# Kernel optimization log

Hardware: AMD Instinct MI355X
Metric: run time of the kernel (lower is better)

The kernel has to match this reference:

```python
import jax, jax.numpy as jnp
import numpy as np

B, T, C = 2, 2048, 2048
N_HEAD = 16
HD = C // N_HEAD  # 128


def setup_inputs() -> dict:
    key = jax.random.key(0)
    k1, k2, k3, k4, k5 = jax.random.split(key, 5)
    s_in = 1.0 / np.sqrt(C)
    return {
        "x": jax.random.normal(k1, (B, T, C), dtype=jnp.float32),
        # weights stored as (in, out), i.e. transpose of torch Linear weight
        "W_attn": jax.random.normal(k2, (C, 3 * C), dtype=jnp.float32) * s_in,
        "b_attn": jax.random.normal(k3, (3 * C,), dtype=jnp.float32) * 0.02,
        "W_proj": jax.random.normal(k4, (C, C), dtype=jnp.float32) * s_in,
        "b_proj": jax.random.normal(k5, (C,), dtype=jnp.float32) * 0.02,
    }


def reference(x, W_attn, b_attn, W_proj, b_proj):
    # qkv projection: (B,T,3C)
    qkv = x @ W_attn + b_attn
    q, k, v = jnp.split(qkv, 3, axis=-1)
    # (B, n_head, T, head_dim)
    q = q.reshape(B, T, N_HEAD, HD).transpose(0, 2, 1, 3)
    k = k.reshape(B, T, N_HEAD, HD).transpose(0, 2, 1, 3)
    v = v.reshape(B, T, N_HEAD, HD).transpose(0, 2, 1, 3)
    # scores (B,H,T,T), causal mask (T_q == T_k prefill path)
    att = jnp.einsum("bhqd,bhkd->bhqk", q, k) * (1.0 / np.sqrt(HD))
    causal = jnp.tril(jnp.ones((T, T), dtype=bool))
    att = jnp.where(causal[None, None], att, -jnp.inf)
    att = jax.nn.softmax(att, axis=-1)  # attn_dropout is identity (p=0)
    y = jnp.einsum("bhqk,bhkd->bhqd", att, v)
    y = y.transpose(0, 2, 1, 3).reshape(B, T, C)
    y = y @ W_proj + b_proj  # resid_dropout identity (p=0)
    # new_cache = (k, v, T) since T == block_size; return output tensor
    return y
```

## Files before the change

### kernel.cpp

```cpp
#include <hip/hip_runtime.h>
#include <cstdint>
#include <cstddef>


typedef __bf16 bf16x8 __attribute__((ext_vector_type(8)));
typedef float  f32x4  __attribute__((ext_vector_type(4)));
typedef unsigned short u16x4 __attribute__((ext_vector_type(4)));
typedef unsigned short u16x8 __attribute__((ext_vector_type(8)));

__device__ __forceinline__ unsigned short f2bf(float f) {
  unsigned int u = __builtin_bit_cast(unsigned int, f);
  u += 0x7fffu + ((u >> 16) & 1u);
  return (unsigned short)(u >> 16);
}

__device__ __forceinline__ void gld16(void* lds, const void* g) {
  __builtin_amdgcn_global_load_lds(
      (const __attribute__((address_space(1))) void*)g,
      (__attribute__((address_space(3))) void*)lds, 16, 0, 0);
}

__device__ __forceinline__ unsigned lds_addr(const void* p) {
  return (unsigned)(size_t)(const __attribute__((address_space(3))) void*)p;
}

__device__ __forceinline__ bf16x8 ds_read16(unsigned addr) {
  bf16x8 r;
  asm volatile("ds_read_b128 %0, %1" : "=v"(r) : "v"(addr));
  return r;
}

__device__ __forceinline__ void ds_write8(unsigned addr, u16x4 d) {
  unsigned long long v = __builtin_bit_cast(unsigned long long, d);
  asm volatile("ds_write_b64 %0, %1" :: "v"(addr), "v"(v));
}

__device__ __forceinline__ void transpose_tile_64(
    const float* __restrict__ in, unsigned short* __restrict__ out,
    int R, int C, int c0, int r0, int t, float tile[64][65]) {
  int lr = t >> 4, lc = (t & 15) * 4;
#pragma unroll
  for (int i = 0; i < 4; i++) {
    int row = lr + i * 16;
    float4 v = *(const float4*)&in[(size_t)(r0 + row) * C + c0 + lc];
    tile[row][lc] = v.x; tile[row][lc + 1] = v.y;
    tile[row][lc + 2] = v.z; tile[row][lc + 3] = v.w;
  }
  __syncthreads();
  int wr = t >> 3, wc = (t & 7) * 8;
#pragma unroll
  for (int i = 0; i < 2; i++) {
    int crow = wr + i * 32;
    u16x8 o;
#pragma unroll
    for (int j = 0; j < 8; j++) o[j] = f2bf(tile[wc + j][crow]);
    *(u16x8*)&out[(size_t)(c0 + crow) * R + r0 + wc] = o;
  }
}

__global__ __launch_bounds__(256) void prep_k(
    const float* __restrict__ x, const float* __restrict__ W_attn,
    const float* __restrict__ W_proj, unsigned short* __restrict__ x_bf,
    unsigned short* __restrict__ WaT, unsigned short* __restrict__ WpT) {
  __shared__ float tile[64][65];
  const int bid = blockIdx.x, t = threadIdx.x;
  if (bid < 3072) {
    int bx = bid % 96, by = bid / 96;
    transpose_tile_64(W_attn, WaT, 2048, 6144, bx * 64, by * 64, t, tile);
  } else if (bid < 4096) {
    int id = bid - 3072, bx = id & 31, by = id >> 5;
    transpose_tile_64(W_proj, WpT, 2048, 2048, bx * 64, by * 64, t, tile);
  } else {
    const int n4 = 8388608 / 4;
    int i = (bid - 4096) * 256 + t;
    for (; i < n4; i += 1024 * 256) {
      float4 v = ((const float4*)x)[i];
      ushort4 o;
      o.x = f2bf(v.x); o.y = f2bf(v.y); o.z = f2bf(v.z); o.w = f2bf(v.w);
      ((ushort4*)x_bf)[i] = o;
    }
  }
}

__global__ __launch_bounds__(256) void extract_vT_k(
    const unsigned short* __restrict__ qkv, unsigned short* __restrict__ vT) {
  __shared__ unsigned int tile32[64][33];
  int bh = blockIdx.z, b = bh >> 4, h = bh & 15;
  int t0 = blockIdx.x * 64, d0 = blockIdx.y * 64;
  int t = threadIdx.x;
  int lr = t >> 3, lc = (t & 7) * 8;
  const unsigned short* src = qkv + (size_t)(b * 2048) * 6144 + 4096 + h * 128;
#pragma unroll
  for (int i = 0; i < 2; i++) {
    int row = lr + i * 32;
    u16x8 v = *(const u16x8*)&src[(size_t)(t0 + row) * 6144 + d0 + lc];
#pragma unroll
    for (int j = 0; j < 8; j++) {
      unsigned short* p = (unsigned short*)&tile32[lc + j][row & 31];
      p[row >> 5] = v[j];
    }
  }
  __syncthreads();
  int dr = t >> 2, tc = (t & 3) * 8;
  u16x8 lo, hi;
#pragma unroll
  for (int j = 0; j < 8; j++) {
    unsigned int u = tile32[dr][tc + j];
    lo[j] = (unsigned short)(u & 0xffffu);
    hi[j] = (unsigned short)(u >> 16);
  }
  unsigned short* dst = vT + (size_t)bh * 128 * 2048 + (size_t)(d0 + dr) * 2048 + t0;
  *(u16x8*)&dst[tc] = lo;
  *(u16x8*)&dst[tc + 32] = hi;
}

template <int OUT_BF16>
__global__ __launch_bounds__(256) void gemm_bt(
    const unsigned short* __restrict__ A, const unsigned short* __restrict__ BT,
    const float* __restrict__ bias, void* __restrict__ Cout,
    int M, int N, int K) {
  __shared__ __align__(16) unsigned short sA[128 * 64];
  __shared__ __align__(16) unsigned short sB[128 * 64];

  const int tid = threadIdx.x, w = tid >> 6, lane = tid & 63;
  const int quad = lane >> 4, l16 = lane & 15;
  const int m0 = blockIdx.y * 128, n0 = blockIdx.x * 128;
  const int wr = w >> 1, wc = w & 1;

  const unsigned short* gA[4];
  const unsigned short* gB[4];
  unsigned short* lA[4];
  unsigned short* lB[4];
#pragma unroll
  for (int i = 0; i < 4; i++) {
    int c = w * 256 + i * 64 + lane;
    int row = c >> 3, scol = (c & 7) ^ (row & 7);
    gA[i] = A + (size_t)(m0 + row) * K + scol * 8;
    gB[i] = BT + (size_t)(n0 + row) * K + scol * 8;
    lA[i] = sA + (size_t)(w * 256 + i * 64) * 8;
    lB[i] = sB + (size_t)(w * 256 + i * 64) * 8;
  }

  f32x4 acc[4][4] = {};

  for (int k0 = 0; k0 < K; k0 += 64) {
#pragma unroll
    for (int i = 0; i < 4; i++) {
      gld16(lA[i], gA[i]); gld16(lB[i], gB[i]);
      gA[i] += 64; gB[i] += 64;
    }
    __syncthreads();

#pragma unroll
    for (int kk = 0; kk < 2; kk++) {
      const int cc = (kk * 4 + quad) ^ (l16 & 7);
      bf16x8 af[4], bfr[4];
#pragma unroll
      for (int mi = 0; mi < 4; mi++)
        af[mi] = *(const bf16x8*)&sA[(wr * 64 + mi * 16 + l16) * 64 + cc * 8];
#pragma unroll
      for (int ni = 0; ni < 4; ni++)
        bfr[ni] = *(const bf16x8*)&sB[(wc * 64 + ni * 16 + l16) * 64 + cc * 8];
#pragma unroll
      for (int mi = 0; mi < 4; mi++)
#pragma unroll
        for (int ni = 0; ni < 4; ni++)
          acc[mi][ni] = __builtin_amdgcn_mfma_f32_16x16x32_bf16(
              af[mi], bfr[ni], acc[mi][ni], 0, 0, 0);
    }
    __syncthreads();
  }

#pragma unroll
  for (int mi = 0; mi < 4; mi++) {
    int row = m0 + wr * 64 + mi * 16 + quad * 4;
#pragma unroll
    for (int ni = 0; ni < 4; ni++) {
      int col = n0 + wc * 64 + ni * 16 + l16;
      float bv = bias[col];
#pragma unroll
      for (int r = 0; r < 4; r++) {
        float v = acc[mi][ni][r] + bv;
        if (OUT_BF16)
          ((unsigned short*)Cout)[(size_t)(row + r) * N + col] = f2bf(v);
        else
          ((float*)Cout)[(size_t)(row + r) * N + col] = v;
      }
    }
  }
}

#define BARRIER8 __builtin_amdgcn_s_barrier()
#define WAIT_LGKM0 asm volatile("s_waitcnt lgkmcnt(0)" ::: "memory")
#define WAIT_LGKM4 asm volatile("s_waitcnt lgkmcnt(4)" ::: "memory")
#define WAIT_LGKM5 asm volatile("s_waitcnt lgkmcnt(5)" ::: "memory")
#define SCHED0 __builtin_amdgcn_sched_barrier(0)
#define WAIT_VM4 asm volatile("s_waitcnt vmcnt(4)" ::: "memory")
#define WAIT_VM0 asm volatile("s_waitcnt vmcnt(0)" ::: "memory")

#define STAGE_A(buf, h, t)                                                   \
  do {                                                                       \
    gld16(&sA[buf][((h) * 1024 + w * 64) * 8],                               \
          gA0 + (size_t)(h) * 128 * K + (size_t)(t) * 64);                   \
    gld16(&sA[buf][((h) * 1024 + 512 + w * 64) * 8],                         \
          gA1 + (size_t)(h) * 128 * K + (size_t)(t) * 64);                   \
  } while (0)

#define STAGE_B(buf, h, t)                                                   \
  do {                                                                       \
    gld16(&sB[buf][((h) * 1024 + w * 64) * 8],                               \
          gB0 + (size_t)(h) * 128 * K + (size_t)(t) * 64);                   \
    gld16(&sB[buf][((h) * 1024 + 512 + w * 64) * 8],                         \
          gB1 + (size_t)(h) * 128 * K + (size_t)(t) * 64);                   \
  } while (0)

#define LDA4(buf, mh, kk)                                                    \
  do {                                                                       \
    const int cc_ = ((kk) * 4 + quad) ^ (l16 & 7);                           \
    _Pragma("unroll") for (int i_ = 0; i_ < 4; ++i_) {                       \
      const int rr_ = (mh) * 128 + wr * 64 + i_ * 16 + l16;                  \
      a_[i_] = ds_read16(lds_addr(&sA[buf][rr_ * 64 + cc_ * 8]));            \
    }                                                                        \
  } while (0)

#define LDB4(buf, kk)                                                        \
  do {                                                                       \
    const int cc_ = ((kk) * 4 + quad) ^ (l16 & 7);                           \
    _Pragma("unroll") for (int i_ = 0; i_ < 4; ++i_) {                       \
      const int rr_ = wc * 64 + i_ * 16 + l16;                               \
      b_[i_] = ds_read16(lds_addr(&sB[buf][rr_ * 64 + cc_ * 8]));            \
    }                                                                        \
  } while (0)

#define MM16(mh)                                                             \
  do {                                                                       \
    __builtin_amdgcn_s_setprio(1);                                           \
    _Pragma("unroll") for (int i_ = 0; i_ < 4; ++i_)                         \
    _Pragma("unroll") for (int n_ = 0; n_ < 4; ++n_)                         \
        acc[(mh) * 4 + i_][n_] = __builtin_amdgcn_mfma_f32_16x16x32_bf16(    \
            a_[i_], b_[n_], acc[(mh) * 4 + i_][n_], 0, 0, 0);                \
    __builtin_amdgcn_s_setprio(0);                                           \
  } while (0)

template <int OUT_BF16>
__global__ __launch_bounds__(512, 2) void gemm_bt8(
    const unsigned short* __restrict__ A, const unsigned short* __restrict__ BT,
    const float* __restrict__ bias, void* __restrict__ Cout,
    int M, int N, int K) {
  __shared__ __align__(16) unsigned short sA[2][256 * 64];
  __shared__ __align__(16) unsigned short sB[2][256 * 64];
  (void)M;

  const int tid = threadIdx.x, w = tid >> 6, lane = tid & 63;
  const int quad = lane >> 4, l16 = lane & 15;
  const int wr = w >> 2, wc = w & 3;

  const int nwgx = gridDim.x;
  const int nwg = nwgx * gridDim.y;
  const int wg = blockIdx.y * nwgx + blockIdx.x;
  const int q8 = nwg >> 3, r8 = nwg & 7;
  const int xcd = wg & 7, loc = wg >> 3;
  const int swz =
      (xcd < r8 ? xcd * (q8 + 1) : r8 * (q8 + 1) + (xcd - r8) * q8) + loc;
  const int m0 = (swz / nwgx) * 256;
  const int n0 = (swz % nwgx) * 256;

  const int c0 = tid, c1 = tid + 512;
  const int r0c = c0 >> 3, s0c = (c0 & 7) ^ (r0c & 7);
  const int r1c = c1 >> 3, s1c = (c1 & 7) ^ (r1c & 7);
  const unsigned short* gA0 = A + (size_t)(m0 + r0c) * K + s0c * 8;
  const unsigned short* gA1 = A + (size_t)(m0 + r1c) * K + s1c * 8;
  const unsigned short* gB0 = BT + (size_t)(n0 + r0c) * K + s0c * 8;
  const unsigned short* gB1 = BT + (size_t)(n0 + r1c) * K + s1c * 8;

  f32x4 acc[8][4] = {};
  bf16x8 a_[4], b_[4];

  const int NT = K >> 6;
  const int NI = NT >> 1;

  STAGE_B(0, 0, 0); STAGE_A(0, 0, 0);
  STAGE_B(0, 1, 0); STAGE_A(0, 1, 0);
  STAGE_B(1, 0, 1); STAGE_A(1, 0, 1);
  WAIT_VM4;
  BARRIER8;

  for (int i = 0; i < NI; ++i) {
    const int t1 = 2 * i + 1;
    const int tn0 = 2 * i + 2, tn1 = 2 * i + 3;
    const bool last = (i == NI - 1);

    LDB4(0, 0); LDA4(0, 0, 0);
    STAGE_B(1, 1, t1); STAGE_A(1, 1, t1);
    BARRIER8; WAIT_LGKM0; SCHED0; MM16(0); BARRIER8;

    LDA4(0, 1, 0);
    BARRIER8; WAIT_LGKM0; SCHED0; MM16(1); BARRIER8;

    LDB4(0, 1); LDA4(0, 0, 1);
    BARRIER8; WAIT_LGKM0; SCHED0; MM16(0); BARRIER8;

    LDA4(0, 1, 1);
    if (!last) {
      STAGE_B(0, 0, tn0); STAGE_A(0, 0, tn0);
      WAIT_VM4;
    } else {
      WAIT_VM0;
    }
    BARRIER8; WAIT_LGKM0; SCHED0; MM16(1); BARRIER8;

    LDB4(1, 0); LDA4(1, 0, 0);
    if (!last) { STAGE_B(0, 1, tn0); STAGE_A(0, 1, tn0); }
    BARRIER8; WAIT_LGKM0; SCHED0; MM16(0); BARRIER8;

    LDA4(1, 1, 0);
    BARRIER8; WAIT_LGKM0; SCHED0; MM16(1); BARRIER8;

    LDB4(1, 1); LDA4(1, 0, 1);
    BARRIER8; WAIT_LGKM0; SCHED0; MM16(0); BARRIER8;

    LDA4(1, 1, 1);
    if (!last) {
      STAGE_B(1, 0, tn1); STAGE_A(1, 0, tn1);
      WAIT_VM4;
    }
    BARRIER8; WAIT_LGKM0; SCHED0; MM16(1); BARRIER8;
  }

#pragma unroll
  for (int mi = 0; mi < 8; ++mi) {
    const int mh = mi >> 2, i2 = mi & 3;
    int row = m0 + mh * 128 + wr * 64 + i2 * 16 + quad * 4;
#pragma unroll
    for (int ni = 0; ni < 4; ++ni) {
      int col = n0 + wc * 64 + ni * 16 + l16;
      float bv = bias[col];
#pragma unroll
      for (int rr = 0; rr < 4; ++rr) {
        float v = acc[mi][ni][rr] + bv;
        if (OUT_BF16)
          ((unsigned short*)Cout)[(size_t)(row + rr) * N + col] = f2bf(v);
        else
          ((float*)Cout)[(size_t)(row + rr) * N + col] = v;
      }
    }
  }
}

#undef STAGE_A
#undef STAGE_B
#undef LDA4
#undef LDB4
#undef MM16

__global__ __launch_bounds__(256) void flash_attn(
    const unsigned short* __restrict__ qkv, const unsigned short* __restrict__ vT,
    unsigned short* __restrict__ yout) {
  __shared__ __align__(16) unsigned short sK[2][64 * 128];
  __shared__ __align__(16) unsigned short sVT[2][128 * 64];
  __shared__ __align__(16) unsigned short sP[4 * 16 * 64];

  const int tid = threadIdx.x, w = tid >> 6, lane = tid & 63;
  const int quad = lane >> 4, l16 = lane & 15;
  const int id = blockIdx.x;
  const int g = id & 31;
  const int qp = id >> 5;
  const int b = g >> 4, h = g & 15;
  const int T = 2048, CC = 6144, HD = 128;
  const float qscale = 0.12753257252f;

  const unsigned short* gK = qkv + (size_t)(b * T) * CC + 2048 + h * HD;
  const unsigned short* gV = vT + (size_t)(b * 16 + h) * HD * T;
  unsigned short* pw = sP + w * 16 * 64;

  const unsigned short* kSrc[4];
  const unsigned short* vSrc[4];
  unsigned short* kDst[4];
  unsigned short* vDst[4];
#pragma unroll
  for (int i = 0; i < 4; i++) {
    int c = w * 256 + i * 64 + lane;
    int kR = c >> 4, kC = (c & 15) ^ (kR & 15);
    int vR = c >> 3, vC = (c & 7) ^ (vR & 7);
    kSrc[i] = gK + (size_t)kR * CC + kC * 8;
    vSrc[i] = gV + (size_t)vR * T + vC * 8;
    kDst[i] = (unsigned short*)sK + (size_t)(w * 256 + i * 64) * 8;
    vDst[i] = (unsigned short*)sVT + (size_t)(w * 256 + i * 64) * 8;
  }
  const int KBUF = 64 * 128, VBUF = 128 * 64;

  const int qtA = qp, qtB = 31 - qp;
  int qt = qtA, kt = 0;

  bf16x8 qf[4];
  float m_old, l_sum;
  f32x4 o[8] = {};
  {
    const size_t qrow = (size_t)(b * T + qt * 64 + w * 16 + l16) * CC + h * HD;
#pragma unroll
    for (int kb = 0; kb < 4; kb++) {
      bf16x8 raw = *(const bf16x8*)&qkv[qrow + kb * 32 + quad * 8];
      bf16x8 sc;
#pragma unroll
      for (int j = 0; j < 8; j++) sc[j] = (__bf16)((float)raw[j] * qscale);
      qf[kb] = sc;
    }
  }
  m_old = -1e30f; l_sum = 0.f;

#pragma unroll
  for (int i = 0; i < 4; i++) {
    gld16(kDst[i], kSrc[i]);
    gld16(vDst[i], vSrc[i]);
  }

  const int total = qtA + qtB + 2;
  for (int it = 0; it < total; ++it) {
    __syncthreads();
    const int cur = it & 1;
    const bool segEnd = (kt == qt);

    if (it + 1 < total) {
      const int nkt = segEnd ? 0 : kt + 1;
      const int nb_ = (it + 1) & 1;
      const size_t kOff = (size_t)nkt * 64 * CC;
      const int vOff = nkt * 64;
#pragma unroll
      for (int i = 0; i < 4; i++) {
        gld16(kDst[i] + (size_t)nb_ * KBUF, kSrc[i] + kOff);
        gld16(vDst[i] + (size_t)nb_ * VBUF, vSrc[i] + vOff);
      }
    }

    const unsigned short* sKc = (const unsigned short*)sK + (size_t)cur * KBUF;
    const unsigned short* sVc = (const unsigned short*)sVT + (size_t)cur * VBUF;

    f32x4 s4[4] = {};
    bf16x8 kf[4], kg[4];
#pragma unroll
    for (int kb = 0; kb < 4; kb++) {
      int rr = kb * 16 + l16;
      int cc = quad ^ l16;
      kf[kb] = ds_read16(lds_addr(&sKc[rr * 128 + cc * 8]));
    }
#pragma unroll
    for (int dc = 0; dc < 4; dc++) {
      if (dc < 3) {
#pragma unroll
        for (int kb = 0; kb < 4; kb++) {
          int rr = kb * 16 + l16;
          int cc = ((dc + 1) * 4 + quad) ^ l16;
          kg[kb] = ds_read16(lds_addr(&sKc[rr * 128 + cc * 8]));
        }
        WAIT_LGKM4;
      } else {
        WAIT_LGKM0;
      }
      SCHED0;
      __builtin_amdgcn_s_setprio(1);
#pragma unroll
      for (int kb = 0; kb < 4; kb++)
        s4[kb] = __builtin_amdgcn_mfma_f32_16x16x32_bf16(kf[kb], qf[dc], s4[kb], 0, 0, 0);
      __builtin_amdgcn_s_setprio(0);
      if (dc < 3) {
#pragma unroll
        for (int kb = 0; kb < 4; kb++) kf[kb] = kg[kb];
      }
    }

    float sv[4][4];
#pragma unroll
    for (int kb = 0; kb < 4; kb++)
#pragma unroll
      for (int r = 0; r < 4; r++) {
        float v = s4[kb][r];
        if (segEnd) {
          if (kb * 16 + quad * 4 + r > w * 16 + l16) v = -1e30f;
        }
        sv[kb][r] = v;
      }

    float mx = sv[0][0];
#pragma unroll
    for (int kb = 0; kb < 4; kb++)
#pragma unroll
      for (int r = 0; r < 4; r++) mx = fmaxf(mx, sv[kb][r]);
    mx = fmaxf(mx, __shfl_xor(mx, 16));
    mx = fmaxf(mx, __shfl_xor(mx, 32));
    float m_new = fmaxf(m_old, mx);
    const bool nogrow = (__all(mx <= m_old + 8.0f) != 0);
    if (nogrow) m_new = m_old;
    float ssum = 0.f;
#pragma unroll
    for (int kb = 0; kb < 4; kb++)
#pragma unroll
      for (int r = 0; r < 4; r++) {
        float p = exp2f(sv[kb][r] - m_new);
        sv[kb][r] = p;
        ssum += p;
      }
    ssum += __shfl_xor(ssum, 16);
    ssum += __shfl_xor(ssum, 32);
    if (nogrow) {
      l_sum += ssum;
    } else {
      float a = exp2f(m_old - m_new);
      float ar[4];
#pragma unroll
      for (int r = 0; r < 4; r++)
        ar[r] = __shfl(a, (lane & 48) + quad * 4 + r);
#pragma unroll
      for (int nb = 0; nb < 8; nb++)
#pragma unroll
        for (int r = 0; r < 4; r++) o[nb][r] *= ar[r];
      l_sum = l_sum * a + ssum;
    }
    m_old = m_new;

#pragma unroll
    for (int kb = 0; kb < 4; kb++) {
      u16x4 pk;
#pragma unroll
      for (int r = 0; r < 4; r++) pk[r] = f2bf(sv[kb][r]);
      int c = kb * 2 + (quad >> 1);
      int cp = c ^ (l16 & 7);
      ds_write8(lds_addr(&pw[l16 * 64 + cp * 8 + (quad & 1) * 4]), pk);
    }
    WAIT_LGKM0;
    SCHED0;

    {
      const int x7 = l16 & 7;
      const int ccP0 = quad ^ x7, ccP1 = (4 + quad) ^ x7;
      bf16x8 pf0, pf1, vA[4], vB[4];
      pf0 = ds_read16(lds_addr(&pw[l16 * 64 + ccP0 * 8]));
#pragma unroll
      for (int j = 0; j < 4; j++) {
        int rr = j * 16 + l16;
        vA[j] = ds_read16(lds_addr(&sVc[rr * 64 + ccP0 * 8]));
      }
#pragma unroll
      for (int j = 0; j < 4; j++) {
        int rr = (4 + j) * 16 + l16;
        vB[j] = ds_read16(lds_addr(&sVc[rr * 64 + ccP0 * 8]));
      }
      WAIT_LGKM4; SCHED0;
      __builtin_amdgcn_s_setprio(1);
#pragma unroll
      for (int j = 0; j < 4; j++)
        o[j] = __builtin_amdgcn_mfma_f32_16x16x32_bf16(pf0, vA[j], o[j], 0, 0, 0);
      __builtin_amdgcn_s_setprio(0);
      pf1 = ds_read16(lds_addr(&pw[l16 * 64 + ccP1 * 8]));
#pragma unroll
      for (int j = 0; j < 4; j++) {
        int rr = j * 16 + l16;
        vA[j] = ds_read16(lds_addr(&sVc[rr * 64 + ccP1 * 8]));
      }
      WAIT_LGKM5; SCHED0;
      __builtin_amdgcn_s_setprio(1);
#pragma unroll
      for (int j = 0; j < 4; j++)
        o[4 + j] = __builtin_amdgcn_mfma_f32_16x16x32_bf16(pf0, vB[j], o[4 + j], 0, 0, 0);
      __builtin_amdgcn_s_setprio(0);
#pragma unroll
      for (int j = 0; j < 4; j++) {
        int rr = (4 + j) * 16 + l16;
        vB[j] = ds_read16(lds_addr(&sVc[rr * 64 + ccP1 * 8]));
      }
      WAIT_LGKM4; SCHED0;
      __builtin_amdgcn_s_setprio(1);
#pragma unroll
      for (int j = 0; j < 4; j++)
        o[j] = __builtin_amdgcn_mfma_f32_16x16x32_bf16(pf1, vA[j], o[j], 0, 0, 0);
      __builtin_amdgcn_s_setprio(0);
      WAIT_LGKM0; SCHED0;
      __builtin_amdgcn_s_setprio(1);
#pragma unroll
      for (int j = 0; j < 4; j++)
        o[4 + j] = __builtin_amdgcn_mfma_f32_16x16x32_bf16(pf1, vB[j], o[4 + j], 0, 0, 0);
      __builtin_amdgcn_s_setprio(0);
    }

    if (segEnd) {
      float linv = 1.0f / l_sum;
#pragma unroll
      for (int r = 0; r < 4; r++) {
        float ir = __shfl(linv, (lane & 48) + quad * 4 + r);
        size_t orow = (size_t)(b * T + qt * 64 + w * 16 + quad * 4 + r) * 2048 + h * HD;
#pragma unroll
        for (int nb = 0; nb < 8; nb++)
          yout[orow + nb * 16 + l16] = f2bf(o[nb][r] * ir);
      }
      if (it + 1 < total) {
        qt = qtB;
        const size_t qrow = (size_t)(b * T + qt * 64 + w * 16 + l16) * CC + h * HD;
#pragma unroll
        for (int kb = 0; kb < 4; kb++) {
          bf16x8 raw = *(const bf16x8*)&qkv[qrow + kb * 32 + quad * 8];
          bf16x8 sc;
#pragma unroll
          for (int j = 0; j < 8; j++) sc[j] = (__bf16)((float)raw[j] * qscale);
          qf[kb] = sc;
        }
        m_old = -1e30f; l_sum = 0.f;
#pragma unroll
        for (int nb = 0; nb < 8; nb++) o[nb] = (f32x4){0.f, 0.f, 0.f, 0.f};
      }
      kt = 0;
    } else {
      kt++;
    }
  }
}

extern "C" void kernel_launch(void* const* d_in, const int* in_sizes, int n_in,
                              void* d_out, int out_size, void* d_ws, size_t ws_size,
                              hipStream_t stream) {
  const float* x      = (const float*)d_in[0];
  const float* W_attn = (const float*)d_in[1];
  const float* b_attn = (const float*)d_in[2];
  const float* W_proj = (const float*)d_in[3];
  const float* b_proj = (const float*)d_in[4];
  float* out = (float*)d_out;

  char* ws = (char*)d_ws;
  unsigned short* x_bf  = (unsigned short*)(ws);
  unsigned short* WaT   = (unsigned short*)(ws + 16777216);
  unsigned short* WpT   = (unsigned short*)(ws + 41943040);
  unsigned short* qkv   = (unsigned short*)(ws + 50331648);
  unsigned short* vT    = (unsigned short*)(ws + 100663296);
  unsigned short* y_att = (unsigned short*)(ws + 117440512);

  prep_k<<<5120, 256, 0, stream>>>(x, W_attn, W_proj, x_bf, WaT, WpT);
  gemm_bt8<1><<<dim3(24, 16), 512, 0, stream>>>(x_bf, WaT, b_attn, qkv, 4096, 6144, 2048);
  extract_vT_k<<<dim3(32, 2, 32), 256, 0, stream>>>(qkv, vT);
  flash_attn<<<dim3(512), 256, 0, stream>>>(qkv, vT, y_att);
  gemm_bt<0><<<dim3(16, 32), 256, 0, stream>>>(y_att, WpT, b_proj, out, 4096, 2048, 2048);
}
```

Before: 369.9 us.

## Fuse V transpose into QKV GEMM epilogue and double-buffer output projection GEMM

The QKV GEMM epilogue now writes the V columns straight into the transposed vT layout as packed 4-element stores, which removes the separate extract_vT kernel and its extra read and write of V. The output projection GEMM is replaced by a double-buffered variant. It prefetches two K-tiles ahead with global_load_lds, uses explicit ds_read and waitcnt scheduling, and raises wave priority around the MFMA blocks. In exchange, the V columns are no longer written to the qkv buffer, and the transposed stores are strided 8-byte writes that may coalesce poorly.

```diff
diff --git a/kernel.cpp b/kernel.cpp
--- a/kernel.cpp
+++ b/kernel.cpp
@@ -34,6 +34,16 @@
   unsigned long long v = __builtin_bit_cast(unsigned long long, d);
   asm volatile("ds_write_b64 %0, %1" :: "v"(addr), "v"(v));
 }
+
+#define BARRIER8 __builtin_amdgcn_s_barrier()
+#define WAIT_LGKM0 asm volatile("s_waitcnt lgkmcnt(0)" ::: "memory")
+#define WAIT_LGKM4 asm volatile("s_waitcnt lgkmcnt(4)" ::: "memory")
+#define WAIT_LGKM5 asm volatile("s_waitcnt lgkmcnt(5)" ::: "memory")
+#define WAIT_LGKM8 asm volatile("s_waitcnt lgkmcnt(8)" ::: "memory")
+#define SCHED0 __builtin_amdgcn_sched_barrier(0)
+#define WAIT_VM4 asm volatile("s_waitcnt vmcnt(4)" ::: "memory")
+#define WAIT_VM8 asm volatile("s_waitcnt vmcnt(8)" ::: "memory")
+#define WAIT_VM0 asm volatile("s_waitcnt vmcnt(0)" ::: "memory")
 
 __device__ __forceinline__ void transpose_tile_64(
     const float* __restrict__ in, unsigned short* __restrict__ out,
@@ -82,122 +92,6 @@
   }
 }
 
-__global__ __launch_bounds__(256) void extract_vT_k(
-    const unsigned short* __restrict__ qkv, unsigned short* __restrict__ vT) {
-  __shared__ unsigned int tile32[64][33];
-  int bh = blockIdx.z, b = bh >> 4, h = bh & 15;
-  int t0 = blockIdx.x * 64, d0 = blockIdx.y * 64;
-  int t = threadIdx.x;
-  int lr = t >> 3, lc = (t & 7) * 8;
-  const unsigned short* src = qkv + (size_t)(b * 2048) * 6144 + 4096 + h * 128;
-#pragma unroll
-  for (int i = 0; i < 2; i++) {
-    int row = lr + i * 32;
-    u16x8 v = *(const u16x8*)&src[(size_t)(t0 + row) * 6144 + d0 + lc];
-#pragma unroll
-    for (int j = 0; j < 8; j++) {
-      unsigned short* p = (unsigned short*)&tile32[lc + j][row & 31];
-      p[row >> 5] = v[j];
-    }
-  }
-  __syncthreads();
-  int dr = t >> 2, tc = (t & 3) * 8;
-  u16x8 lo, hi;
-#pragma unroll
-  for (int j = 0; j < 8; j++) {
-    unsigned int u = tile32[dr][tc + j];
-    lo[j] = (unsigned short)(u & 0xffffu);
-    hi[j] = (unsigned short)(u >> 16);
-  }
-  unsigned short* dst = vT + (size_t)bh * 128 * 2048 + (size_t)(d0 + dr) * 2048 + t0;
-  *(u16x8*)&dst[tc] = lo;
-  *(u16x8*)&dst[tc + 32] = hi;
-}
-
-template <int OUT_BF16>
-__global__ __launch_bounds__(256) void gemm_bt(
-    const unsigned short* __restrict__ A, const unsigned short* __restrict__ BT,
-    const float* __restrict__ bias, void* __restrict__ Cout,
-    int M, int N, int K) {
-  __shared__ __align__(16) unsigned short sA[128 * 64];
-  __shared__ __align__(16) unsigned short sB[128 * 64];
-
-  const int tid = threadIdx.x, w = tid >> 6, lane = tid & 63;
-  const int quad = lane >> 4, l16 = lane & 15;
-  const int m0 = blockIdx.y * 128, n0 = blockIdx.x * 128;
-  const int wr = w >> 1, wc = w & 1;
-
-  const unsigned short* gA[4];
-  const unsigned short* gB[4];
-  unsigned short* lA[4];
-  unsigned short* lB[4];
-#pragma unroll
-  for (int i = 0; i < 4; i++) {
-    int c = w * 256 + i * 64 + lane;
-    int row = c >> 3, scol = (c & 7) ^ (row & 7);
-    gA[i] = A + (size_t)(m0 + row) * K + scol * 8;
-    gB[i] = BT + (size_t)(n0 + row) * K + scol * 8;
-    lA[i] = sA + (size_t)(w * 256 + i * 64) * 8;
-    lB[i] = sB + (size_t)(w * 256 + i * 64) * 8;
-  }
-
-  f32x4 acc[4][4] = {};
-
-  for (int k0 = 0; k0 < K; k0 += 64) {
-#pragma unroll
-    for (int i = 0; i < 4; i++) {
-      gld16(lA[i], gA[i]); gld16(lB[i], gB[i]);
-      gA[i] += 64; gB[i] += 64;
-    }
-    __syncthreads();
-
-#pragma unroll
-    for (int kk = 0; kk < 2; kk++) {
-      const int cc = (kk * 4 + quad) ^ (l16 & 7);
-      bf16x8 af[4], bfr[4];
-#pragma unroll
-      for (int mi = 0; mi < 4; mi++)
-        af[mi] = *(const bf16x8*)&sA[(wr * 64 + mi * 16 + l16) * 64 + cc * 8];
-#pragma unroll
-      for (int ni = 0; ni < 4; ni++)
-        bfr[ni] = *(const bf16x8*)&sB[(wc * 64 + ni * 16 + l16) * 64 + cc * 8];
-#pragma unroll
-      for (int mi = 0; mi < 4; mi++)
-#pragma unroll
-        for (int ni = 0; ni < 4; ni++)
-          acc[mi][ni] = __builtin_amdgcn_mfma_f32_16x16x32_bf16(
-              af[mi], bfr[ni], acc[mi][ni], 0, 0, 0);
-    }
-    __syncthreads();
-  }
-
-#pragma unroll
-  for (int mi = 0; mi < 4; mi++) {
-    int row = m0 + wr * 64 + mi * 16 + quad * 4;
-#pragma unroll
-    for (int ni = 0; ni < 4; ni++) {
-      int col = n0 + wc * 64 + ni * 16 + l16;
-      float bv = bias[col];
-#pragma unroll
-      for (int r = 0; r < 4; r++) {
-        float v = acc[mi][ni][r] + bv;
-        if (OUT_BF16)
-          ((unsigned short*)Cout)[(size_t)(row + r) * N + col] = f2bf(v);
-        else
-          ((float*)Cout)[(size_t)(row + r) * N + col] = v;
-      }
-    }
-  }
-}
-
-#define BARRIER8 __builtin_amdgcn_s_barrier()
-#define WAIT_LGKM0 asm volatile("s_waitcnt lgkmcnt(0)" ::: "memory")
-#define WAIT_LGKM4 asm volatile("s_waitcnt lgkmcnt(4)" ::: "memory")
-#define WAIT_LGKM5 asm volatile("s_waitcnt lgkmcnt(5)" ::: "memory")
-#define SCHED0 __builtin_amdgcn_sched_barrier(0)
-#define WAIT_VM4 asm volatile("s_waitcnt vmcnt(4)" ::: "memory")
-#define WAIT_VM0 asm volatile("s_waitcnt vmcnt(0)" ::: "memory")
-
 #define STAGE_A(buf, h, t)                                                   \
   do {                                                                       \
     gld16(&sA[buf][((h) * 1024 + w * 64) * 8],                               \
@@ -246,6 +140,7 @@
 __global__ __launch_bounds__(512, 2) void gemm_bt8(
     const unsigned short* __restrict__ A, const unsigned short* __restrict__ BT,
     const float* __restrict__ bias, void* __restrict__ Cout,
+    unsigned short* __restrict__ vTout,
     int M, int N, int K) {
   __shared__ __align__(16) unsigned short sA[2][256 * 64];
   __shared__ __align__(16) unsigned short sB[2][256 * 64];
@@ -327,21 +222,41 @@
     BARRIER8; WAIT_LGKM0; SCHED0; MM16(1); BARRIER8;
   }
 
-#pragma unroll
-  for (int mi = 0; mi < 8; ++mi) {
-    const int mh = mi >> 2, i2 = mi & 3;
-    int row = m0 + mh * 128 + wr * 64 + i2 * 16 + quad * 4;
-#pragma unroll
-    for (int ni = 0; ni < 4; ++ni) {
-      int col = n0 + wc * 64 + ni * 16 + l16;
-      float bv = bias[col];
-#pragma unroll
-      for (int rr = 0; rr < 4; ++rr) {
-        float v = acc[mi][ni][rr] + bv;
-        if (OUT_BF16)
-          ((unsigned short*)Cout)[(size_t)(row + rr) * N + col] = f2bf(v);
-        else
-          ((float*)Cout)[(size_t)(row + rr) * N + col] = v;
+  if (OUT_BF16 && n0 >= 4096) {
+#pragma unroll
+    for (int mi = 0; mi < 8; ++mi) {
+      const int mh = mi >> 2, i2 = mi & 3;
+      const int grow = m0 + mh * 128 + wr * 64 + i2 * 16 + quad * 4;
+      const int bb = grow >> 11, tt = grow & 2047;
+      unsigned short* vbase = vTout + (size_t)bb * 2048 * 2048 + tt;
+#pragma unroll
+      for (int ni = 0; ni < 4; ++ni) {
+        const int col = n0 + wc * 64 + ni * 16 + l16;
+        const float bv = bias[col];
+        const int vcol = col - 4096;
+        u16x4 pk;
+#pragma unroll
+        for (int rr = 0; rr < 4; ++rr) pk[rr] = f2bf(acc[mi][ni][rr] + bv);
+        *(u16x4*)&vbase[(size_t)vcol * 2048] = pk;
+      }
+    }
+  } else {
+#pragma unroll
+    for (int mi = 0; mi < 8; ++mi) {
+      const int mh = mi >> 2, i2 = mi & 3;
+      int row = m0 + mh * 128 + wr * 64 + i2 * 16 + quad * 4;
+#pragma unroll
+      for (int ni = 0; ni < 4; ++ni) {
+        int col = n0 + wc * 64 + ni * 16 + l16;
+        float bv = bias[col];
+#pragma unroll
+        for (int rr = 0; rr < 4; ++rr) {
+          float v = acc[mi][ni][rr] + bv;
+          if (OUT_BF16)
+            ((unsigned short*)Cout)[(size_t)(row + rr) * N + col] = f2bf(v);
+          else
+            ((float*)Cout)[(size_t)(row + rr) * N + col] = v;
+        }
       }
     }
   }
@@ -352,6 +267,116 @@
 #undef LDA4
 #undef LDB4
 #undef MM16
+
+template <int OUT_BF16>
+__global__ __launch_bounds__(256) void gemm_db(
+    const unsigned short* __restrict__ A, const unsigned short* __restrict__ BT,
+    const float* __restrict__ bias, void* __restrict__ Cout,
+    int M, int N, int K) {
+  __shared__ __align__(16) unsigned short sA[2][128 * 64];
+  __shared__ __align__(16) unsigned short sB[2][128 * 64];
+
+  const int tid = threadIdx.x, w = tid >> 6, lane = tid & 63;
+  const int quad = lane >> 4, l16 = lane & 15;
+  const int m0 = blockIdx.y * 128, n0 = blockIdx.x * 128;
+  const int wr = w >> 1, wc = w & 1;
+
+  const unsigned short* gA[4];
+  const unsigned short* gB[4];
+  unsigned aOff[4];
+#pragma unroll
+  for (int i = 0; i < 4; i++) {
+    int c = w * 256 + i * 64 + lane;
+    int row = c >> 3, scol = (c & 7) ^ (row & 7);
+    gA[i] = A + (size_t)(m0 + row) * K + scol * 8;
+    gB[i] = BT + (size_t)(n0 + row) * K + scol * 8;
+    aOff[i] = (unsigned)((w * 256 + i * 64) * 8);
+  }
+
+  f32x4 acc[4][4] = {};
+  const int NT = K >> 6;
+
+#pragma unroll
+  for (int i = 0; i < 4; i++) { gld16(&sA[0][aOff[i]], gA[i]); gld16(&sB[0][aOff[i]], gB[i]); }
+#pragma unroll
+  for (int i = 0; i < 4; i++) { gld16(&sA[1][aOff[i]], gA[i] + 64); gld16(&sB[1][aOff[i]], gB[i] + 64); }
+  WAIT_VM8;
+  BARRIER8;
+
+  bf16x8 a0_[4], b0_[4], a1_[4], b1_[4];
+  for (int t = 0; t < NT; ++t) {
+    const int c = t & 1;
+    const int cc0 = quad ^ (l16 & 7);
+    const int cc1 = (4 + quad) ^ (l16 & 7);
+#pragma unroll
+    for (int i = 0; i < 4; i++)
+      b0_[i] = ds_read16(lds_addr(&sB[c][(wc * 64 + i * 16 + l16) * 64 + cc0 * 8]));
+#pragma unroll
+    for (int i = 0; i < 4; i++)
+      a0_[i] = ds_read16(lds_addr(&sA[c][(wr * 64 + i * 16 + l16) * 64 + cc0 * 8]));
+#pragma unroll
+    for (int i = 0; i < 4; i++)
+      b1_[i] = ds_read16(lds_addr(&sB[c][(wc * 64 + i * 16 + l16) * 64 + cc1 * 8]));
+#pragma unroll
+    for (int i = 0; i < 4; i++)
+      a1_[i] = ds_read16(lds_addr(&sA[c][(wr * 64 + i * 16 + l16) * 64 + cc1 * 8]));
+
+    WAIT_LGKM8; SCHED0;
+    __builtin_amdgcn_s_setprio(1);
+#pragma unroll
+    for (int mi = 0; mi < 4; mi++)
+#pragma unroll
+      for (int ni = 0; ni < 4; ni++)
+        acc[mi][ni] = __builtin_amdgcn_mfma_f32_16x16x32_bf16(
+            a0_[mi], b0_[ni], acc[mi][ni], 0, 0, 0);
+    __builtin_amdgcn_s_setprio(0);
+
+    WAIT_LGKM0; SCHED0;
+    BARRIER8;
+
+    if (t + 2 < NT) {
+#pragma unroll
+      for (int i = 0; i < 4; i++) {
+        gld16(&sA[c][aOff[i]], gA[i] + (size_t)(t + 2) * 64);
+        gld16(&sB[c][aOff[i]], gB[i] + (size_t)(t + 2) * 64);
+      }
+    }
+
+    __builtin_amdgcn_s_setprio(1);
+#pragma unroll
+    for (int mi = 0; mi < 4; mi++)
+#pragma unroll
+      for (int ni = 0; ni < 4; ni++)
+        acc[mi][ni] = __builtin_amdgcn_mfma_f32_16x16x32_bf16(
+            a1_[mi], b1_[ni], acc[mi][ni], 0, 0, 0);
+    __builtin_amdgcn_s_setprio(0);
+
+    if (t + 2 < NT) {
+      WAIT_VM8;
+    } else if (t + 1 < NT) {
+      WAIT_VM0;
+    }
+    BARRIER8;
+  }
+
+#pragma unroll
+  for (int mi = 0; mi < 4; mi++) {
+    int row = m0 + wr * 64 + mi * 16 + quad * 4;
+#pragma unroll
+    for (int ni = 0; ni < 4; ni++) {
+      int col = n0 + wc * 64 + ni * 16 + l16;
+      float bv = bias[col];
+#pragma unroll
+      for (int r = 0; r < 4; r++) {
+        float v = acc[mi][ni][r] + bv;
+        if (OUT_BF16)
+          ((unsigned short*)Cout)[(size_t)(row + r) * N + col] = f2bf(v);
+        else
+          ((float*)Cout)[(size_t)(row + r) * N + col] = v;
+      }
+    }
+  }
+}
 
 __global__ __launch_bounds__(256) void flash_attn(
     const unsigned short* __restrict__ qkv, const unsigned short* __restrict__ vT,
@@ -632,8 +657,7 @@
   unsigned short* y_att = (unsigned short*)(ws + 117440512);
 
   prep_k<<<5120, 256, 0, stream>>>(x, W_attn, W_proj, x_bf, WaT, WpT);
-  gemm_bt8<1><<<dim3(24, 16), 512, 0, stream>>>(x_bf, WaT, b_attn, qkv, 4096, 6144, 2048);
-  extract_vT_k<<<dim3(32, 2, 32), 256, 0, stream>>>(qkv, vT);
+  gemm_bt8<1><<<dim3(24, 16), 512, 0, stream>>>(x_bf, WaT, b_attn, qkv, vT, 4096, 6144, 2048);
   flash_attn<<<dim3(512), 256, 0, stream>>>(qkv, vT, y_att);
-  gemm_bt<0><<<dim3(16, 32), 256, 0, stream>>>(y_att, WpT, b_proj, out, 4096, 2048, 2048);
-}
+  gemm_db<0><<<dim3(16, 32), 256, 0, stream>>>(y_att, WpT, b_proj, out, 4096, 2048, 2048);
+}
```

Result: no change. 369.8 us (-0.0%).
